# Performance work log

Measured on AMD Instinct MI355X. Metric: run time of the kernel, lower is better.

## Reference

```python
import jax, jax.numpy as jnp
import numpy as np

B, S, H, L = 2, 192, 768, 4

def setup_inputs() -> dict:
    key = jax.random.key(0)
    ks = jax.random.split(key, 6)
    scale = 1.0 / np.sqrt(H)
    return {
        "pooled": jax.random.normal(ks[0], (B, S, H), dtype=jnp.float32),
        "W_src": jax.random.normal(ks[1], (H * L, H), dtype=jnp.float32) * scale,
        "b_src": jax.random.normal(ks[2], (H * L,), dtype=jnp.float32) * 0.02,
        "W_tgt": jax.random.normal(ks[3], (H * L, H), dtype=jnp.float32) * scale,
        "b_tgt": jax.random.normal(ks[4], (H * L,), dtype=jnp.float32) * 0.02,
        "classifier_weight": jax.random.normal(ks[5], (H, L), dtype=jnp.float32) * scale,
    }

def reference(pooled, W_src, b_src, W_tgt, b_tgt, classifier_weight):
    b, s, h = pooled.shape
    l = classifier_weight.shape[1]
    # Linear projections: (b,s,h) @ (h, L*h) -> (b,s,L,h)
    h_source = (pooled @ W_src.T + b_src).reshape(b, s, l, h)
    h_target = (pooled @ W_tgt.T + b_tgt).reshape(b, s, l, h)
    # Pairwise broadcast-add -> (b,s,t,l,h), exact (erf) GELU as in nn.GELU()
    hidden = jax.nn.gelu(h_source[:, :, None] + h_target[:, None], approximate=False)
    # dropout is identity at inference
    return jnp.einsum('bstlh,hl->bstl', hidden, classifier_weight)
```

## Files before the change

### kernel.cpp

```cpp
#include <hip/hip_runtime.h>
#include <math.h>

#define BQ 2
#define SQ 192
#define HQ 768
#define LQ 4

typedef float f2    __attribute__((ext_vector_type(2)));
typedef float f32x4 __attribute__((ext_vector_type(4)));
typedef short bf16x8 __attribute__((ext_vector_type(8)));

__device__ __forceinline__ f2 gelu2(f2 x) {
  f2 ax = __builtin_elementwise_abs(x);
  f2 q  = __builtin_elementwise_fma((f2)0.0232217f, ax, (f2)0.00040867f);
  q     = __builtin_elementwise_fma(q, ax, (f2)0.1369901f);
  q     = __builtin_elementwise_fma(q, ax, (f2)0.2340973f);
  q     = __builtin_elementwise_fma(q, ax, (f2)1.18920712f);
  f2 r;
  r.x = __builtin_amdgcn_rcpf(q.x);
  r.y = __builtin_amdgcn_rcpf(q.y);
  f2 r2 = r * r;
  f2 r4 = r2 * r2;
  f2 relu = __builtin_elementwise_max(x, (f2)0.0f);
  return __builtin_elementwise_fma(-ax, r4, relu);
}

__device__ __forceinline__ unsigned short bf16_rne(float x) {
  unsigned u = __float_as_uint(x);
  return (unsigned short)((u + 0x7fffu + ((u >> 16) & 1u)) >> 16);
}

__global__ __launch_bounds__(256) void prep_kernel(
    const float* __restrict__ pooled, const float* __restrict__ Ws,
    const float* __restrict__ Wt, const float* __restrict__ cw,
    unsigned short* __restrict__ Ab, unsigned short* __restrict__ Wsb,
    unsigned short* __restrict__ Wtb, float* __restrict__ clp)
{
  const int NAq = (BQ * SQ * HQ) / 4;
  const int NWq = (LQ * HQ * HQ) / 4;
  const int total = NAq + 2 * NWq;
  int gid = blockIdx.x * 256 + threadIdx.x;
  if (gid < LQ * HQ) {
    int l = gid / HQ, h = gid % HQ;
    clp[gid] = cw[h * LQ + l];
  }
  for (int i = gid; i < total; i += gridDim.x * 256) {
    const float* src; unsigned short* dst; int j;
    if (i < NAq)            { src = pooled; dst = Ab;  j = i; }
    else if (i < NAq + NWq) { src = Ws;     dst = Wsb; j = i - NAq; }
    else                    { src = Wt;     dst = Wtb; j = i - NAq - NWq; }
    float4 v = *(const float4*)&src[(size_t)j * 4];
    ushort4 o;
    o.x = bf16_rne(v.x); o.y = bf16_rne(v.y);
    o.z = bf16_rne(v.z); o.w = bf16_rne(v.w);
    *(ushort4*)&dst[(size_t)j * 4] = o;
  }
}

__global__ __launch_bounds__(256) void proj_mfma(
    const unsigned short* __restrict__ Ab,
    const unsigned short* __restrict__ Wsb, const unsigned short* __restrict__ Wtb,
    const float* __restrict__ b0, const float* __restrict__ b1,
    float* __restrict__ o0, float* __restrict__ o1)
{
  int id  = blockIdx.x + 6 * (blockIdx.y + 48 * blockIdx.z);
  int nid = (id & 7) * 72 + (id >> 3);
  int bx = nid % 6, by = (nid / 6) % 48, bz = nid / 288;

  const unsigned short* W = bz ? Wtb : Wsb;
  const float* bias = bz ? b1 : b0;
  float* out        = bz ? o1 : o0;

  int tid  = threadIdx.x;
  int w    = tid >> 6;
  int lane = tid & 63;
  int wm = w >> 1, wn = w & 1;
  int m_base = bx * 64 + wm * 32;
  int n_base = by * 64 + wn * 32;
  int r = lane & 15, g = lane >> 4;

  const unsigned short* a0p = Ab + (size_t)(m_base + r) * HQ + g * 8;
  const unsigned short* a1p = a0p + 16 * HQ;
  const unsigned short* w0p = W + (size_t)(n_base + r) * HQ + g * 8;
  const unsigned short* w1p = w0p + 16 * HQ;

  f32x4 acc00 = {0,0,0,0}, acc01 = {0,0,0,0}, acc10 = {0,0,0,0}, acc11 = {0,0,0,0};

  bf16x8 a0 = *(const bf16x8*)a0p, a1 = *(const bf16x8*)a1p;
  bf16x8 v0 = *(const bf16x8*)w0p, v1 = *(const bf16x8*)w1p;
  for (int kt = 0; kt < 23; ++kt) {
    int off = (kt + 1) * 32;
    bf16x8 na0 = *(const bf16x8*)(a0p + off), na1 = *(const bf16x8*)(a1p + off);
    bf16x8 nv0 = *(const bf16x8*)(w0p + off), nv1 = *(const bf16x8*)(w1p + off);
    acc00 = __builtin_amdgcn_mfma_f32_16x16x32_bf16(a0, v0, acc00, 0, 0, 0);
    acc01 = __builtin_amdgcn_mfma_f32_16x16x32_bf16(a0, v1, acc01, 0, 0, 0);
    acc10 = __builtin_amdgcn_mfma_f32_16x16x32_bf16(a1, v0, acc10, 0, 0, 0);
    acc11 = __builtin_amdgcn_mfma_f32_16x16x32_bf16(a1, v1, acc11, 0, 0, 0);
    a0 = na0; a1 = na1; v0 = nv0; v1 = nv1;
  }
  acc00 = __builtin_amdgcn_mfma_f32_16x16x32_bf16(a0, v0, acc00, 0, 0, 0);
  acc01 = __builtin_amdgcn_mfma_f32_16x16x32_bf16(a0, v1, acc01, 0, 0, 0);
  acc10 = __builtin_amdgcn_mfma_f32_16x16x32_bf16(a1, v0, acc10, 0, 0, 0);
  acc11 = __builtin_amdgcn_mfma_f32_16x16x32_bf16(a1, v1, acc11, 0, 0, 0);

  int l      = n_base / HQ;
  int h_base = n_base % HQ;
  int bb     = m_base / SQ;
  int c      = lane & 15;
  float bv0 = bias[n_base + c];
  float bv1 = bias[n_base + 16 + c];
  #pragma unroll
  for (int i = 0; i < 2; ++i) {
    f32x4 A0 = i ? acc10 : acc00;
    f32x4 A1 = i ? acc11 : acc01;
    #pragma unroll
    for (int reg = 0; reg < 4; ++reg) {
      int m = m_base + i * 16 + g * 4 + reg;
      int s = m - bb * SQ;
      float* op = out + (((size_t)(bb * LQ + l) * SQ + s) * HQ) + h_base;
      op[c]      = A0[reg] + bv0;
      op[16 + c] = A1[reg] + bv1;
    }
  }
}

__global__ __launch_bounds__(256) void proj_kernel(
    const float* __restrict__ A,
    const float* __restrict__ W0, const float* __restrict__ b0,
    const float* __restrict__ W1, const float* __restrict__ b1,
    float* __restrict__ o0, float* __restrict__ o1)
{
  const float* W  = blockIdx.z ? W1 : W0;
  const float* bs = blockIdx.z ? b1 : b0;
  float* out      = blockIdx.z ? o1 : o0;

  __shared__ float As[32][68];
  __shared__ float Wt[64][68];

  const int tid = threadIdx.x;
  const int tx  = tid & 15;
  const int ty  = tid >> 4;
  const int m0  = blockIdx.x * 32;
  const int n0  = blockIdx.y * 64;

  const int ar[2] = { (tid + 0) >> 4, (tid + 256) >> 4 };
  const int ac    = (tid & 15) << 2;
  const int wr[4] = { tid >> 4, (tid + 256) >> 4, (tid + 512) >> 4, (tid + 768) >> 4 };
  const int wc    = (tid & 15) << 2;

  float4 pa[2], pw[4];
  #pragma unroll
  for (int i = 0; i < 2; ++i)
    pa[i] = *(const float4*)&A[(size_t)(m0 + ar[i]) * HQ + ac];
  #pragma unroll
  for (int i = 0; i < 4; ++i)
    pw[i] = *(const float4*)&W[(size_t)(n0 + wr[i]) * HQ + wc];

  float acc[2][4];
  #pragma unroll
  for (int j = 0; j < 2; ++j)
    #pragma unroll
    for (int n = 0; n < 4; ++n) acc[j][n] = 0.f;

  for (int kt = 0; kt < 12; ++kt) {
    __syncthreads();
    #pragma unroll
    for (int i = 0; i < 2; ++i)
      *(float4*)&As[ar[i]][ac] = pa[i];
    #pragma unroll
    for (int i = 0; i < 4; ++i) {
      Wt[wc + 0][wr[i]] = pw[i].x; Wt[wc + 1][wr[i]] = pw[i].y;
      Wt[wc + 2][wr[i]] = pw[i].z; Wt[wc + 3][wr[i]] = pw[i].w;
    }
    if (kt < 11) {
      int ko = (kt + 1) * 64;
      #pragma unroll
      for (int i = 0; i < 2; ++i)
        pa[i] = *(const float4*)&A[(size_t)(m0 + ar[i]) * HQ + ko + ac];
      #pragma unroll
      for (int i = 0; i < 4; ++i)
        pw[i] = *(const float4*)&W[(size_t)(n0 + wr[i]) * HQ + ko + wc];
    }
    __syncthreads();

    #pragma unroll
    for (int kk = 0; kk < 64; kk += 4) {
      float4 a[2], wv[4];
      #pragma unroll
      for (int j = 0; j < 2; ++j)
        a[j] = *(float4*)&As[2 * ty + j][kk];
      #pragma unroll
      for (int i = 0; i < 4; ++i)
        wv[i] = *(float4*)&Wt[kk + i][4 * tx];
      #pragma unroll
      for (int i = 0; i < 4; ++i) {
        #pragma unroll
        for (int j = 0; j < 2; ++j) {
          float av = ((const float*)&a[j])[i];
          acc[j][0] = fmaf(av, wv[i].x, acc[j][0]);
          acc[j][1] = fmaf(av, wv[i].y, acc[j][1]);
          acc[j][2] = fmaf(av, wv[i].z, acc[j][2]);
          acc[j][3] = fmaf(av, wv[i].w, acc[j][3]);
        }
      }
    }
  }

  const int l  = n0 / HQ;
  const int h0 = n0 % HQ;
  float4 bv = *(const float4*)&bs[n0 + 4 * tx];
  #pragma unroll
  for (int j = 0; j < 2; ++j) {
    int m  = m0 + 2 * ty + j;
    int bb = m / SQ, s = m % SQ;
    float4 v;
    v.x = acc[j][0] + bv.x; v.y = acc[j][1] + bv.y;
    v.z = acc[j][2] + bv.z; v.w = acc[j][3] + bv.w;
    *(float4*)(out + (((size_t)(bb * LQ + l) * SQ + s) * HQ) + h0 + 4 * tx) = v;
  }
}

__global__ __launch_bounds__(256) void pack_kernel(const float* __restrict__ cw,
                                                   float* __restrict__ clp) {
  int i = blockIdx.x * 256 + threadIdx.x;
  int l = i / HQ, h = i % HQ;
  clp[i] = cw[h * LQ + l];
}

__global__ __launch_bounds__(256) void pair_kernel(
    const float* __restrict__ hsrc, const float* __restrict__ htgt,
    const float* __restrict__ clp, float* __restrict__ out)
{
  int id  = blockIdx.x + 12 * (blockIdx.y + 12 * blockIdx.z);
  int nid = (id & 7) * 144 + (id >> 3);
  int bix = nid % 12, biy = (nid / 12) % 12, bl = nid / 144;

  const int bb = bl >> 2, l = bl & 3;
  const int s0 = bix * 16;
  const int t0 = biy * 16;
  const int tid = threadIdx.x;
  const int tt = tid & 15;
  const int ts = tid >> 4;

  __shared__ float hs[16][260];
  __shared__ float ht[16][260];

  const float* hs_g  = hsrc + ((size_t)bl * SQ + s0) * HQ;
  const float* ht_g  = htgt + ((size_t)bl * SQ + t0) * HQ;
  const float* clp_l = clp + l * HQ;

  f2 acc = {0.f, 0.f};
  for (int ck = 0; ck < 3; ++ck) {
    __syncthreads();
    #pragma unroll
    for (int i = 0; i < 4; ++i) {
      int f4 = tid + i * 256;
      int r  = f4 >> 6;
      int c  = (f4 & 63) << 2;
      *(float4*)&hs[r][c] = *(const float4*)&hs_g[(size_t)r * HQ + ck * 256 + c];
    }
    #pragma unroll
    for (int i = 0; i < 4; ++i) {
      int f4 = tid + i * 256;
      int r  = f4 >> 6;
      int c  = (f4 & 63) << 2;
      *(float4*)&ht[r][c] = *(const float4*)&ht_g[(size_t)r * HQ + ck * 256 + c];
    }
    __syncthreads();

    #pragma unroll 4
    for (int k = 0; k < 256; k += 4) {
      float4 a  = *(float4*)&hs[ts][k];
      float4 b  = *(float4*)&ht[tt][k];
      float4 c4 = *(const float4*)&clp_l[ck * 256 + k];
      const f2* ap = (const f2*)&a;
      const f2* bp = (const f2*)&b;
      const f2* cp = (const f2*)&c4;
      acc = __builtin_elementwise_fma(gelu2(ap[0] + bp[0]), cp[0], acc);
      acc = __builtin_elementwise_fma(gelu2(ap[1] + bp[1]), cp[1], acc);
    }
  }

  out[(((size_t)bb * SQ + (s0 + ts)) * SQ + (t0 + tt)) * LQ + l] = acc.x + acc.y;
}

extern "C" void kernel_launch(void* const* d_in, const int* in_sizes, int n_in,
                              void* d_out, int out_size, void* d_ws, size_t ws_size,
                              hipStream_t stream) {
  const float* pooled = (const float*)d_in[0];
  const float* Wsrc   = (const float*)d_in[1];
  const float* bsrc   = (const float*)d_in[2];
  const float* Wtgt   = (const float*)d_in[3];
  const float* btgt   = (const float*)d_in[4];
  const float* cw     = (const float*)d_in[5];
  float* out = (float*)d_out;

  const size_t nhs = (size_t)BQ * LQ * SQ * HQ;
  float* clp = (float*)d_ws;
  float* hs  = clp + LQ * HQ;
  float* ht  = hs + nhs;
  unsigned short* Ab  = (unsigned short*)(ht + nhs);
  unsigned short* Wsb = Ab + (size_t)BQ * SQ * HQ;
  unsigned short* Wtb = Wsb + (size_t)LQ * HQ * HQ;

  size_t need_full = (size_t)(LQ * HQ + 2 * nhs) * 4 +
                     (size_t)(BQ * SQ * HQ + 2 * LQ * HQ * HQ) * 2;

  if (ws_size >= need_full) {
    prep_kernel<<<dim3(1024), 256, 0, stream>>>(pooled, Wsrc, Wtgt, cw, Ab, Wsb, Wtb, clp);
    proj_mfma<<<dim3(6, 48, 2), 256, 0, stream>>>(Ab, Wsb, Wtb, bsrc, btgt, hs, ht);
  } else {
    pack_kernel<<<dim3(12), 256, 0, stream>>>(cw, clp);
    proj_kernel<<<dim3(12, 48, 2), 256, 0, stream>>>(pooled, Wsrc, bsrc, Wtgt, btgt, hs, ht);
  }
  pair_kernel<<<dim3(12, 12, 8), 256, 0, stream>>>(hs, ht, clp, out);
}
```

Measured before the change: 177.8 us.

## Pre-pack bf16 operands in MFMA fragment order and slim pair kernel LDS

The prep kernel now writes pooled and both weight matrices in an MFMA-fragment-packed layout, so each lane of the projection GEMM loads a contiguous 16-byte chunk. The GEMM becomes one-wave blocks over a larger grid. The pair kernel drops the source tile from LDS and reads each thread's source row straight from global memory. It keeps only an XOR-swizzled target tile, uses scalar GELU with four accumulation chains collapsed into one, and sets an occupancy hint. These changes aim to cut uncoalesced loads, LDS traffic and bank conflicts, at the cost of more redundant global reads of source rows and a serialized accumulation chain.

```diff
diff --git a/kernel.cpp b/kernel.cpp
--- a/kernel.cpp
+++ b/kernel.cpp
@@ -6,23 +6,17 @@
 #define HQ 768
 #define LQ 4
 
-typedef float f2    __attribute__((ext_vector_type(2)));
 typedef float f32x4 __attribute__((ext_vector_type(4)));
 typedef short bf16x8 __attribute__((ext_vector_type(8)));
 
-__device__ __forceinline__ f2 gelu2(f2 x) {
-  f2 ax = __builtin_elementwise_abs(x);
-  f2 q  = __builtin_elementwise_fma((f2)0.0232217f, ax, (f2)0.00040867f);
-  q     = __builtin_elementwise_fma(q, ax, (f2)0.1369901f);
-  q     = __builtin_elementwise_fma(q, ax, (f2)0.2340973f);
-  q     = __builtin_elementwise_fma(q, ax, (f2)1.18920712f);
-  f2 r;
-  r.x = __builtin_amdgcn_rcpf(q.x);
-  r.y = __builtin_amdgcn_rcpf(q.y);
-  f2 r2 = r * r;
-  f2 r4 = r2 * r2;
-  f2 relu = __builtin_elementwise_max(x, (f2)0.0f);
-  return __builtin_elementwise_fma(-ax, r4, relu);
+__device__ __forceinline__ float gelu_f(float x) {
+  float ax = fabsf(x);
+  float q = fmaf(fmaf(fmaf(fmaf(0.0232217f, ax, 0.00040867f), ax, 0.1369901f),
+                      ax, 0.2340973f), ax, 1.18920712f);
+  float r  = __builtin_amdgcn_rcpf(q);
+  float r2 = r * r;
+  float r4 = r2 * r2;
+  return fmaf(-ax, r4, fmaxf(x, 0.f));
 }
 
 __device__ __forceinline__ unsigned short bf16_rne(float x) {
@@ -36,60 +30,66 @@
     unsigned short* __restrict__ Ab, unsigned short* __restrict__ Wsb,
     unsigned short* __restrict__ Wtb, float* __restrict__ clp)
 {
-  const int NAq = (BQ * SQ * HQ) / 4;
-  const int NWq = (LQ * HQ * HQ) / 4;
-  const int total = NAq + 2 * NWq;
-  int gid = blockIdx.x * 256 + threadIdx.x;
-  if (gid < LQ * HQ) {
-    int l = gid / HQ, h = gid % HQ;
-    clp[gid] = cw[h * LQ + l];
-  }
-  for (int i = gid; i < total; i += gridDim.x * 256) {
-    const float* src; unsigned short* dst; int j;
-    if (i < NAq)            { src = pooled; dst = Ab;  j = i; }
-    else if (i < NAq + NWq) { src = Ws;     dst = Wsb; j = i - NAq; }
-    else                    { src = Wt;     dst = Wtb; j = i - NAq - NWq; }
-    float4 v = *(const float4*)&src[(size_t)j * 4];
-    ushort4 o;
-    o.x = bf16_rne(v.x); o.y = bf16_rne(v.y);
-    o.z = bf16_rne(v.z); o.w = bf16_rne(v.w);
-    *(ushort4*)&dst[(size_t)j * 4] = o;
-  }
-}
-
-__global__ __launch_bounds__(256) void proj_mfma(
-    const unsigned short* __restrict__ Ab,
-    const unsigned short* __restrict__ Wsb, const unsigned short* __restrict__ Wtb,
+  int blk = blockIdx.x;
+  if (blk >= 408) {
+    int i = (blk - 408) * 256 + threadIdx.x;
+    clp[i] = cw[(i % HQ) * LQ + i / HQ];
+    return;
+  }
+  const float* src; unsigned short* dst; int rt;
+  if (blk < 24)       { src = pooled; dst = Ab;  rt = blk; }
+  else if (blk < 216) { src = Ws;     dst = Wsb; rt = blk - 24; }
+  else                { src = Wt;     dst = Wtb; rt = blk - 216; }
+
+  #pragma unroll
+  for (int i = 0; i < 6; ++i) {
+    int c    = threadIdx.x + i * 256;
+    int kt   = c >> 6;
+    int lane = c & 63;
+    int row  = rt * 16 + (lane & 15);
+    int col  = kt * 32 + (lane >> 4) * 8;
+    const float* s = src + (size_t)row * HQ + col;
+    float4 v0 = *(const float4*)s;
+    float4 v1 = *(const float4*)(s + 4);
+    ushort4 o0, o1;
+    o0.x = bf16_rne(v0.x); o0.y = bf16_rne(v0.y);
+    o0.z = bf16_rne(v0.z); o0.w = bf16_rne(v0.w);
+    o1.x = bf16_rne(v1.x); o1.y = bf16_rne(v1.y);
+    o1.z = bf16_rne(v1.z); o1.w = bf16_rne(v1.w);
+    unsigned short* d = dst + ((size_t)(rt * 24 + kt) * 64 + lane) * 8;
+    *(ushort4*)d       = o0;
+    *(ushort4*)(d + 4) = o1;
+  }
+}
+
+__global__ __launch_bounds__(64) void proj_mfma(
+    const unsigned short* __restrict__ APk,
+    const unsigned short* __restrict__ WsPk, const unsigned short* __restrict__ WtPk,
     const float* __restrict__ b0, const float* __restrict__ b1,
     float* __restrict__ o0, float* __restrict__ o1)
 {
-  int id  = blockIdx.x + 6 * (blockIdx.y + 48 * blockIdx.z);
-  int nid = (id & 7) * 72 + (id >> 3);
-  int bx = nid % 6, by = (nid / 6) % 48, bz = nid / 288;
-
-  const unsigned short* W = bz ? Wtb : Wsb;
+  int id  = blockIdx.x + 12 * (blockIdx.y + 96 * blockIdx.z);
+  int nid = (id & 7) * 288 + (id >> 3);
+  int bm = nid % 12, bn = (nid / 12) % 96, bz = nid / 1152;
+
+  const unsigned short* WPk = bz ? WtPk : WsPk;
   const float* bias = bz ? b1 : b0;
   float* out        = bz ? o1 : o0;
 
-  int tid  = threadIdx.x;
-  int w    = tid >> 6;
-  int lane = tid & 63;
-  int wm = w >> 1, wn = w & 1;
-  int m_base = bx * 64 + wm * 32;
-  int n_base = by * 64 + wn * 32;
-  int r = lane & 15, g = lane >> 4;
-
-  const unsigned short* a0p = Ab + (size_t)(m_base + r) * HQ + g * 8;
-  const unsigned short* a1p = a0p + 16 * HQ;
-  const unsigned short* w0p = W + (size_t)(n_base + r) * HQ + g * 8;
-  const unsigned short* w1p = w0p + 16 * HQ;
+  int lane = threadIdx.x;
+  int m_base = bm * 32, n_base = bn * 32;
+
+  const unsigned short* a0p = APk + (size_t)(bm * 2) * 24 * 512 + lane * 8;
+  const unsigned short* a1p = a0p + 24 * 512;
+  const unsigned short* w0p = WPk + (size_t)(bn * 2) * 24 * 512 + lane * 8;
+  const unsigned short* w1p = w0p + 24 * 512;
 
   f32x4 acc00 = {0,0,0,0}, acc01 = {0,0,0,0}, acc10 = {0,0,0,0}, acc11 = {0,0,0,0};
 
   bf16x8 a0 = *(const bf16x8*)a0p, a1 = *(const bf16x8*)a1p;
   bf16x8 v0 = *(const bf16x8*)w0p, v1 = *(const bf16x8*)w1p;
   for (int kt = 0; kt < 23; ++kt) {
-    int off = (kt + 1) * 32;
+    int off = (kt + 1) * 512;
     bf16x8 na0 = *(const bf16x8*)(a0p + off), na1 = *(const bf16x8*)(a1p + off);
     bf16x8 nv0 = *(const bf16x8*)(w0p + off), nv1 = *(const bf16x8*)(w1p + off);
     acc00 = __builtin_amdgcn_mfma_f32_16x16x32_bf16(a0, v0, acc00, 0, 0, 0);
@@ -106,7 +106,7 @@
   int l      = n_base / HQ;
   int h_base = n_base % HQ;
   int bb     = m_base / SQ;
-  int c      = lane & 15;
+  int c      = lane & 15, g = lane >> 4;
   float bv0 = bias[n_base + c];
   float bv1 = bias[n_base + 16 + c];
   #pragma unroll
@@ -227,7 +227,7 @@
   clp[i] = cw[h * LQ + l];
 }
 
-__global__ __launch_bounds__(256) void pair_kernel(
+__global__ __launch_bounds__(256, 8) void pair_kernel(
     const float* __restrict__ hsrc, const float* __restrict__ htgt,
     const float* __restrict__ clp, float* __restrict__ out)
 {
@@ -242,46 +242,40 @@
   const int tt = tid & 15;
   const int ts = tid >> 4;
 
-  __shared__ float hs[16][260];
-  __shared__ float ht[16][260];
-
-  const float* hs_g  = hsrc + ((size_t)bl * SQ + s0) * HQ;
-  const float* ht_g  = htgt + ((size_t)bl * SQ + t0) * HQ;
-  const float* clp_l = clp + l * HQ;
-
-  f2 acc = {0.f, 0.f};
+  __shared__ float htile[16][256];
+
+  const float* hs_row = hsrc + ((size_t)bl * SQ + s0 + ts) * HQ;
+  const float* ht_g   = htgt + ((size_t)bl * SQ + t0) * HQ;
+  const float* clp_l  = clp + l * HQ;
+
+  const int tsw = (tt & 7) << 2;
+
+  float acc = 0.f;
   for (int ck = 0; ck < 3; ++ck) {
     __syncthreads();
     #pragma unroll
     for (int i = 0; i < 4; ++i) {
       int f4 = tid + i * 256;
       int r  = f4 >> 6;
-      int c  = (f4 & 63) << 2;
-      *(float4*)&hs[r][c] = *(const float4*)&hs_g[(size_t)r * HQ + ck * 256 + c];
-    }
-    #pragma unroll
-    for (int i = 0; i < 4; ++i) {
-      int f4 = tid + i * 256;
-      int r  = f4 >> 6;
-      int c  = (f4 & 63) << 2;
-      *(float4*)&ht[r][c] = *(const float4*)&ht_g[(size_t)r * HQ + ck * 256 + c];
+      int cq = (f4 & 63) << 2;
+      float4 v = *(const float4*)&ht_g[(size_t)r * HQ + ck * 256 + cq];
+      *(float4*)&htile[r][cq ^ ((r & 7) << 2)] = v;
     }
     __syncthreads();
 
     #pragma unroll 4
     for (int k = 0; k < 256; k += 4) {
-      float4 a  = *(float4*)&hs[ts][k];
-      float4 b  = *(float4*)&ht[tt][k];
+      float4 a  = *(const float4*)&hs_row[ck * 256 + k];
+      float4 b  = *(float4*)&htile[tt][k ^ tsw];
       float4 c4 = *(const float4*)&clp_l[ck * 256 + k];
-      const f2* ap = (const f2*)&a;
-      const f2* bp = (const f2*)&b;
-      const f2* cp = (const f2*)&c4;
-      acc = __builtin_elementwise_fma(gelu2(ap[0] + bp[0]), cp[0], acc);
-      acc = __builtin_elementwise_fma(gelu2(ap[1] + bp[1]), cp[1], acc);
-    }
-  }
-
-  out[(((size_t)bb * SQ + (s0 + ts)) * SQ + (t0 + tt)) * LQ + l] = acc.x + acc.y;
+      acc = fmaf(gelu_f(a.x + b.x), c4.x, acc);
+      acc = fmaf(gelu_f(a.y + b.y), c4.y, acc);
+      acc = fmaf(gelu_f(a.z + b.z), c4.z, acc);
+      acc = fmaf(gelu_f(a.w + b.w), c4.w, acc);
+    }
+  }
+
+  out[(((size_t)bb * SQ + (s0 + ts)) * SQ + (t0 + tt)) * LQ + l] = acc;
 }
 
 extern "C" void kernel_launch(void* const* d_in, const int* in_sizes, int n_in,
@@ -307,8 +301,8 @@
                      (size_t)(BQ * SQ * HQ + 2 * LQ * HQ * HQ) * 2;
 
   if (ws_size >= need_full) {
-    prep_kernel<<<dim3(1024), 256, 0, stream>>>(pooled, Wsrc, Wtgt, cw, Ab, Wsb, Wtb, clp);
-    proj_mfma<<<dim3(6, 48, 2), 256, 0, stream>>>(Ab, Wsb, Wtb, bsrc, btgt, hs, ht);
+    prep_kernel<<<dim3(420), 256, 0, stream>>>(pooled, Wsrc, Wtgt, cw, Ab, Wsb, Wtb, clp);
+    proj_mfma<<<dim3(12, 96, 2), 64, 0, stream>>>(Ab, Wsb, Wtb, bsrc, btgt, hs, ht);
   } else {
     pack_kernel<<<dim3(12), 256, 0, stream>>>(cw, clp);
     proj_kernel<<<dim3(12, 48, 2), 256, 0, stream>>>(pooled, Wsrc, bsrc, Wtgt, btgt, hs, ht);
```

Measured after the change: 174.2 us. 1.02x faster.
